# Optimization experiments

Hardware: AMD Instinct MI355X
Metric: run time of the kernel (lower is better)

The kernel has to match this reference:

```python
import jax, jax.numpy as jnp
import numpy as np

SQRT_DK = jnp.sqrt(jnp.float32(128.0))
BN_EPS = 1e-5


def setup_inputs() -> dict:
    key = jax.random.key(0)
    ks = jax.random.split(key, 12)
    B, C, F, Fp, K, O, DK = 4, 64, 20000, 10000, 16, 128, 128
    fea = jax.random.normal(ks[0], (B, C, F), dtype=jnp.float32)
    ring_n = jax.random.randint(ks[1], (B, Fp, K), 0, F, dtype=jnp.int64)
    pool_idx = jnp.sort(jax.random.randint(ks[2], (Fp,), 0, F, dtype=jnp.int64))
    pos_embed = jnp.zeros((1, 1, 1), dtype=jnp.float32)
    s = 1.0 / np.sqrt(C)
    Wk = jax.random.uniform(ks[3], (DK, C), jnp.float32, -s, s)
    bk = jax.random.uniform(ks[4], (DK,), jnp.float32, -s, s)
    Wq = jax.random.uniform(ks[5], (DK, C), jnp.float32, -s, s)
    bq = jax.random.uniform(ks[6], (DK,), jnp.float32, -s, s)
    Wc = jax.random.uniform(ks[7], (O, C), jnp.float32, -s, s)
    bc = jax.random.uniform(ks[8], (O,), jnp.float32, -s, s)
    gamma = jnp.ones((O,), jnp.float32)
    beta = jnp.zeros((O,), jnp.float32)
    return {"fea": fea, "ring_n": ring_n, "pool_idx": pool_idx, "pos_embed": pos_embed,
            "Wk": Wk, "bk": bk, "Wq": Wq, "bq": bq, "Wc": Wc, "bc": bc,
            "gamma": gamma, "beta": beta}


def _gather_neighbors(fea, ring_n):
    # fea: [B,C,F], ring_n: [B,Fp,K] -> [B,C,Fp,K]
    return jax.vmap(lambda f, r: f[:, r])(fea, ring_n)


def reference(fea, ring_n, pool_idx, pos_embed, Wk, bk, Wq, bq, Wc, bc, gamma, beta):
    # neighbor gather along face dim
    neighbor_fea = _gather_neighbors(fea, ring_n)            # [B,C,Fp,K]
    self_fea = fea[:, :, pool_idx][..., None]                # [B,C,Fp,1]
    cat = jnp.concatenate([self_fea, neighbor_fea], axis=3)  # [B,C,Fp,K+1]
    # per-face key (self only) and per-neighbor query (Linear4D over channel dim)
    keyv = jnp.einsum('bcfk,oc->bofk', self_fea, Wk) + bk[None, :, None, None]  # [B,128,Fp,1]
    query = jnp.einsum('bcfk,oc->bofk', cat, Wq) + bq[None, :, None, None]       # [B,128,Fp,K+1]
    att = jnp.sum(keyv * query, axis=1, keepdims=True) / SQRT_DK                 # [B,1,Fp,K+1]
    att = jax.nn.softmax(att, axis=3)
    agg = jnp.sum(cat * att, axis=3)                                             # [B,C,Fp]
    # concat_mlp: 1x1 conv + BatchNorm1d (training-mode batch stats) + ReLU
    y = jnp.einsum('bcf,oc->bof', agg, Wc) + bc[None, :, None]                   # [B,O,Fp]
    mean = jnp.mean(y, axis=(0, 2), keepdims=True)
    var = jnp.var(y, axis=(0, 2), keepdims=True)
    y = (y - mean) * jax.lax.rsqrt(var + BN_EPS)
    y = y * gamma[None, :, None] + beta[None, :, None]
    return jax.nn.relu(y)
```

## Files before the change

kernel.cpp:

```cpp
#include <hip/hip_runtime.h>

#define F_ALL 20000
#define FP    10000
#define BB    4
#define KK    16
#define OO    128
#define NFACE 40000
#define NBLK  625

#define WS_FEAT 0
#define WS_AGG  (BB*F_ALL*64)
#define WS_GP   (WS_AGG + NFACE*64)
#define WS_SAP  (WS_GP + NBLK*4096)
#define WS_MT   (WS_SAP + NBLK*64)
#define WS_V0   (WS_MT + 4096)
#define WS_G    (WS_V0 + 64)
#define WS_SUMA (WS_G + 4096)
#define WS_SC   (WS_SUMA + 64)
#define WS_SH   (WS_SC + 128)

template<int CTRL>
__device__ __forceinline__ float dpp_add(float x) {
    return x + __int_as_float(__builtin_amdgcn_update_dpp(0, __float_as_int(x), CTRL, 0xF, 0xF, true));
}
__device__ __forceinline__ float sum16(float x) {
    x = dpp_add<0x121>(x);
    x = dpp_add<0x122>(x);
    x = dpp_add<0x124>(x);
    x = dpp_add<0x128>(x);
    return x;
}

__device__ __forceinline__ int swz_tile(int bid) {
    int q = bid & 7, s = bid >> 3;
    return (q == 0) ? s : (79 + (q - 1) * 78 + s);
}

__device__ __forceinline__ unsigned int f2bf(float f) {
    unsigned int u = __float_as_uint(f);
    return (u + 0x7FFFu + ((u >> 16) & 1u)) >> 16;
}
__device__ __forceinline__ float b2f(unsigned short h) {
    return __uint_as_float(((unsigned int)h) << 16);
}
__device__ __forceinline__ void up2(unsigned int v, float* d) {
    d[0] = __uint_as_float((v & 0xFFFFu) << 16);
    d[1] = __uint_as_float(v & 0xFFFF0000u);
}

__global__ __launch_bounds__(256) void k_pre(const float* __restrict__ fea,
                                             const float* __restrict__ Wk,
                                             const float* __restrict__ bk,
                                             const float* __restrict__ Wq,
                                             float* __restrict__ ws) {
    __shared__ float tile[64][65];
    int tid = threadIdx.x;
    if (blockIdx.x < 1252) {
        int bb = blockIdx.x / 313;
        int tb = blockIdx.x % 313;
        int fbase = tb * 64;
        int x  = tid & 63;
        int y0 = tid >> 6;
        int f = fbase + x;
        if (f < F_ALL) {
#pragma unroll
            for (int i = 0; i < 16; i++) {
                int c = y0 + i * 4;
                tile[c][x] = fea[((long)bb * 64 + c) * F_ALL + f];
            }
        }
        __syncthreads();
        unsigned int* feaTh = (unsigned int*)(ws + WS_FEAT);
        int xc = (tid & 31) * 2;
        int yr = tid >> 5;
#pragma unroll
        for (int i = 0; i < 8; i++) {
            int fr = yr + i * 8;
            int ff = fbase + fr;
            if (ff < F_ALL) {
                unsigned int lo = f2bf(tile[xc][fr]);
                unsigned int hi = f2bf(tile[xc + 1][fr]);
                feaTh[(long)(bb * F_ALL + ff) * 32 + (tid & 31)] = lo | (hi << 16);
            }
        }
    } else {
        int idx = (blockIdx.x - 1252) * 256 + tid;
        int j = idx >> 6, i = idx & 63;
        float acc = 0.f;
#pragma unroll 8
        for (int o = 0; o < 128; o++) acc += Wq[o * 64 + i] * Wk[o * 64 + j];
        ws[WS_MT + idx] = acc;
        if (blockIdx.x == 1252 && tid < 64) {
            float a = 0.f;
            for (int o = 0; o < 128; o++) a += Wq[o * 64 + tid] * bk[o];
            ws[WS_V0 + tid] = a;
            ws[WS_SUMA + tid] = 0.f;
        }
    }
}

__global__ __launch_bounds__(256) void k_attn(const int* __restrict__ ring,
                                              const int* __restrict__ pool,
                                              float* __restrict__ ws) {
    __shared__ __align__(16) float lds[4160];
    float* Sf = lds;
    int tid = threadIdx.x;
    int tilei = swz_tile(blockIdx.x);
    int fbase = tilei * 64;
    const unsigned short* feaTh = (const unsigned short*)(ws + WS_FEAT);
    const float* MTg  = ws + WS_MT;
    const float scale = 0.08838834764831845f;

    {
        int r = tid >> 2;
        int face = fbase + r;
        int b = face / FP;
        int p = pool[face - b * FP];
        const uint4* src = (const uint4*)(feaTh + ((long)(b * F_ALL + p)) * 64);
        int q = tid & 3;
        uint4 A  = src[q * 2];
        uint4 Bv = src[q * 2 + 1];
        float* d = &Sf[r * 65 + q * 16];
        up2(A.x,  d +  0); up2(A.y,  d +  2); up2(A.z,  d +  4); up2(A.w,  d +  6);
        up2(Bv.x, d +  8); up2(Bv.y, d + 10); up2(Bv.z, d + 12); up2(Bv.w, d + 14);
    }
    __syncthreads();

    int lane = tid & 63;
    int il = lane & 15, c4 = il * 4;
    int f0 = tid >> 4;

    float4 u[4];
    {
        float4 v0 = *(const float4*)&ws[WS_V0 + c4];
        u[0] = v0; u[1] = v0; u[2] = v0; u[3] = v0;
#pragma unroll 8
        for (int j = 0; j < 64; j++) {
            float4 m4 = *(const float4*)&MTg[j * 64 + c4];
            float a0 = Sf[(f0     ) * 65 + j];
            float a1 = Sf[(f0 + 16) * 65 + j];
            float a2 = Sf[(f0 + 32) * 65 + j];
            float a3 = Sf[(f0 + 48) * 65 + j];
            u[0].x += m4.x * a0; u[0].y += m4.y * a0; u[0].z += m4.z * a0; u[0].w += m4.w * a0;
            u[1].x += m4.x * a1; u[1].y += m4.y * a1; u[1].z += m4.z * a1; u[1].w += m4.w * a1;
            u[2].x += m4.x * a2; u[2].y += m4.y * a2; u[2].z += m4.z * a2; u[2].w += m4.w * a2;
            u[3].x += m4.x * a3; u[3].y += m4.y * a3; u[3].z += m4.z * a3; u[3].w += m4.w * a3;
        }
    }

    float4 a_res[4];
#pragma unroll
    for (int it = 0; it < 4; it++) {
        int fl = f0 + it * 16;
        int face = fbase + fl;
        int b = face / FP;
        const unsigned short* fb = feaTh + (long)b * F_ALL * 64 + c4;

        float4 sf = make_float4(Sf[fl * 65 + c4], Sf[fl * 65 + c4 + 1],
                                Sf[fl * 65 + c4 + 2], Sf[fl * 65 + c4 + 3]);
        float4 uu = u[it];
        int rv = ring[face * KK + il];

        float m = sum16(uu.x * sf.x + uu.y * sf.y + uu.z * sf.z + uu.w * sf.w) * scale;
        float den = 1.f;
        float4 acc = sf;
#pragma unroll
        for (int ch = 0; ch < 2; ch++) {
            float4 nv[8];
#pragma unroll
            for (int k = 0; k < 8; k++) {
                int rk = __shfl(rv, (lane & 48) | (ch * 8 + k), 64);
                ushort4 hv = *(const ushort4*)(fb + (long)rk * 64);
                nv[k] = make_float4(b2f(hv.x), b2f(hv.y), b2f(hv.z), b2f(hv.w));
            }
            float l[8];
#pragma unroll
            for (int k = 0; k < 8; k++)
                l[k] = sum16(uu.x * nv[k].x + uu.y * nv[k].y +
                             uu.z * nv[k].z + uu.w * nv[k].w) * scale;
            float cm = l[0];
#pragma unroll
            for (int k = 1; k < 8; k++) cm = fmaxf(cm, l[k]);
            float nm = fmaxf(m, cm);
            float rs = __expf(m - nm);
            den *= rs;
            acc.x *= rs; acc.y *= rs; acc.z *= rs; acc.w *= rs;
            m = nm;
#pragma unroll
            for (int k = 0; k < 8; k++) {
                float e = __expf(l[k] - m);
                den += e;
                acc.x += e * nv[k].x;
                acc.y += e * nv[k].y;
                acc.z += e * nv[k].z;
                acc.w += e * nv[k].w;
            }
        }
        float inv = 1.0f / den;
        float4 a = make_float4(acc.x * inv, acc.y * inv, acc.z * inv, acc.w * inv);
        a_res[it] = a;
        *(float4*)&ws[WS_AGG + (long)face * 64 + c4] = a;
    }
    __syncthreads();
    float* Ag = lds;
#pragma unroll
    for (int it = 0; it < 4; it++) {
        int fl = f0 + it * 16;
        *(float4*)&Ag[fl * 64 + c4] = a_res[it];
    }
    __syncthreads();

    int ti = tid & 15, tj = tid >> 4;
    float acc[4][4];
#pragma unroll
    for (int a = 0; a < 4; a++)
#pragma unroll
        for (int b = 0; b < 4; b++) acc[a][b] = 0.f;
    float gacc[4] = {0.f, 0.f, 0.f, 0.f};
#pragma unroll 4
    for (int f = 0; f < 64; f++) {
        float4 av = *(const float4*)&Ag[f * 64 + ti * 4];
        float4 bv = *(const float4*)&Ag[f * 64 + tj * 4];
        float avv[4] = {av.x, av.y, av.z, av.w};
        float bvv[4] = {bv.x, bv.y, bv.z, bv.w};
#pragma unroll
        for (int a = 0; a < 4; a++) {
#pragma unroll
            for (int b = 0; b < 4; b++) acc[a][b] += avv[a] * bvv[b];
            gacc[a] += avv[a];
        }
    }
    float* gp = ws + WS_GP;
#pragma unroll
    for (int a = 0; a < 4; a++)
        *(float4*)&gp[(long)tilei * 4096 + (ti * 4 + a) * 64 + tj * 4] =
            make_float4(acc[a][0], acc[a][1], acc[a][2], acc[a][3]);
    if (tj == 0)
        *(float4*)&ws[WS_SAP + tilei * 64 + ti * 4] =
            make_float4(gacc[0], gacc[1], gacc[2], gacc[3]);
}

__global__ __launch_bounds__(256) void k_gsum(float* __restrict__ ws) {
    __shared__ float red[256];
    int t = threadIdx.x;
    if (blockIdx.x < 256) {
        const float* gp = ws + WS_GP;
        int e16 = blockIdx.x * 16;
        int e = t & 15, c = t >> 4;
        int p0 = c * 40;
        int p1 = p0 + 40; if (p1 > NBLK) p1 = NBLK;
        float s0 = 0.f, s1 = 0.f, s2 = 0.f, s3 = 0.f;
        int p = p0;
        for (; p + 4 <= p1; p += 4) {
            s0 += gp[(long)(p + 0) * 4096 + e16 + e];
            s1 += gp[(long)(p + 1) * 4096 + e16 + e];
            s2 += gp[(long)(p + 2) * 4096 + e16 + e];
            s3 += gp[(long)(p + 3) * 4096 + e16 + e];
        }
        for (; p < p1; p++) s0 += gp[(long)p * 4096 + e16 + e];
        red[t] = (s0 + s1) + (s2 + s3);
        __syncthreads();
        if (t < 16) {
            float s = 0.f;
#pragma unroll
            for (int cc = 0; cc < 16; cc++) s += red[cc * 16 + t];
            ws[WS_G + e16 + t] = s;
        }
    } else {
        const float* sap = ws + WS_SAP;
        int bq = blockIdx.x - 256;
        int e = t & 63, c = t >> 6;
        int pidx = bq * 4 + c;
        int p0 = pidx * 40;
        int p1 = p0 + 40; if (p1 > NBLK) p1 = NBLK;
        float s0 = 0.f, s1 = 0.f, s2 = 0.f, s3 = 0.f;
        int p = p0;
        for (; p + 4 <= p1; p += 4) {
            s0 += sap[(p + 0) * 64 + e];
            s1 += sap[(p + 1) * 64 + e];
            s2 += sap[(p + 2) * 64 + e];
            s3 += sap[(p + 3) * 64 + e];
        }
        for (; p < p1; p++) s0 += sap[p * 64 + e];
        red[t] = (s0 + s1) + (s2 + s3);
        __syncthreads();
        if (t < 64) {
            float tot = red[t] + red[t + 64] + red[t + 128] + red[t + 192];
            atomicAdd(&ws[WS_SUMA + t], tot);
        }
    }
}

__global__ __launch_bounds__(256) void k_stats(const float* __restrict__ Wc,
                                               const float* __restrict__ bc,
                                               const float* __restrict__ gamma,
                                               const float* __restrict__ beta,
                                               float* __restrict__ ws) {
    __shared__ float Gs[4096];
    __shared__ float gs[64];
    __shared__ float qs[256];
    int tid = threadIdx.x;
    for (int i = tid; i < 4096; i += 256) Gs[i] = ws[WS_G + i];
    if (tid < 64) gs[tid] = ws[WS_SUMA + tid];
    __syncthreads();

    int o = tid & 127, h = tid >> 7;
    float w[64];
#pragma unroll
    for (int q = 0; q < 16; q++) {
        float4 t = *(const float4*)&Wc[o * 64 + q * 4];
        w[q * 4 + 0] = t.x; w[q * 4 + 1] = t.y; w[q * 4 + 2] = t.z; w[q * 4 + 3] = t.w;
    }
    float qp = 0.f;
    for (int i = h * 32; i < h * 32 + 32; i++) {
        float t = 0.f;
#pragma unroll
        for (int j = 0; j < 64; j++) t += Gs[i * 64 + j] * w[j];
        qp += Wc[o * 64 + i] * t;
    }
    qs[tid] = qp;
    __syncthreads();
    if (h == 0) {
        const float invN = 1.0f / (float)NFACE;
        float qform = qs[o] + qs[o + 128];
        float md = 0.f;
#pragma unroll
        for (int j = 0; j < 64; j++) md += gs[j] * w[j];
        float bco = bc[o];
        float mean = md * invN + bco;
        float ey2  = (qform + 2.f * bco * md) * invN + bco * bco;
        float var  = ey2 - mean * mean;
        float sc   = gamma[o] * rsqrtf(var + 1e-5f);
        ws[WS_SC + o] = sc;
        ws[WS_SH + o] = beta[o] + (bco - mean) * sc;
    }
}

__global__ __launch_bounds__(256) void k_out(const float* __restrict__ Wc,
                                             const float* __restrict__ ws,
                                             float* __restrict__ out) {
    __shared__ __align__(16) float WcT[64 * 132];
    __shared__ __align__(16) float AgT[64 * 68];
    const float* agg = ws + WS_AGG;
    int tid = threadIdx.x;
    int fbase = blockIdx.x * 64;
    for (int i = tid; i < 128 * 64; i += 256) {
        int o = i >> 6, j = i & 63;
        WcT[j * 132 + o] = Wc[i];
    }
    for (int i = tid; i < 64 * 64; i += 256) {
        int f = i >> 6, j = i & 63;
        AgT[j * 68 + f] = agg[((long)(fbase + f)) * 64 + j];
    }
    __syncthreads();

    int tx = tid & 15, ty = tid >> 4;
    float acc[8][4];
#pragma unroll
    for (int a = 0; a < 8; a++)
#pragma unroll
        for (int b = 0; b < 4; b++) acc[a][b] = 0.f;

    for (int j = 0; j < 64; j++) {
        float4 w0 = *(const float4*)&WcT[j * 132 + ty * 8];
        float4 w1 = *(const float4*)&WcT[j * 132 + ty * 8 + 4];
        float4 a0 = *(const float4*)&AgT[j * 68 + tx * 4];
        float wv[8] = {w0.x, w0.y, w0.z, w0.w, w1.x, w1.y, w1.z, w1.w};
        float av[4] = {a0.x, a0.y, a0.z, a0.w};
#pragma unroll
        for (int oi = 0; oi < 8; oi++)
#pragma unroll
            for (int fi = 0; fi < 4; fi++) acc[oi][fi] += wv[oi] * av[fi];
    }

    int fg0 = fbase + tx * 4;
    int b   = fg0 / FP;
    int fp0 = fg0 - b * FP;
#pragma unroll
    for (int oi = 0; oi < 8; oi++) {
        int o = ty * 8 + oi;
        float sc = ws[WS_SC + o];
        float sh = ws[WS_SH + o];
        float4 v;
        v.x = fmaxf(acc[oi][0] * sc + sh, 0.f);
        v.y = fmaxf(acc[oi][1] * sc + sh, 0.f);
        v.z = fmaxf(acc[oi][2] * sc + sh, 0.f);
        v.w = fmaxf(acc[oi][3] * sc + sh, 0.f);
        *(float4*)&out[((long)(b * OO + o)) * FP + fp0] = v;
    }
}

extern "C" void kernel_launch(void* const* d_in, const int* in_sizes, int n_in,
                              void* d_out, int out_size, void* d_ws, size_t ws_size,
                              hipStream_t stream) {
    const float* fea  = (const float*)d_in[0];
    const int*   ring = (const int*)d_in[1];
    const int*   pool = (const int*)d_in[2];
    const float* Wk = (const float*)d_in[4];
    const float* bk = (const float*)d_in[5];
    const float* Wq = (const float*)d_in[6];
    const float* Wc = (const float*)d_in[8];
    const float* bc = (const float*)d_in[9];
    const float* gamma = (const float*)d_in[10];
    const float* beta  = (const float*)d_in[11];

    float* out = (float*)d_out;
    float* ws  = (float*)d_ws;

    k_pre  <<<1268, 256, 0, stream>>>(fea, Wk, bk, Wq, ws);
    k_attn <<<NBLK, 256, 0, stream>>>(ring, pool, ws);
    k_gsum <<<260,  256, 0, stream>>>(ws);
    k_stats<<<1,    256, 0, stream>>>(Wc, bc, gamma, beta, ws);
    k_out  <<<NBLK, 256, 0, stream>>>(Wc, ws, out);
}
```

Measured before the change: 165.2 us.

## Fold BN stats into output kernel, stage MT in LDS, prefetch ring indices

Removes the single-block k_stats launch and has every k_out block recompute the BatchNorm scale and shift from the Gram matrix and channel sums, keeping them in shared memory. In k_attn the 64x64 MT matrix is staged into LDS instead of being read from global memory in the inner loop, and the four ring index loads are issued before the barrier so they overlap with the feature staging. The aim is to drop a serial one-block kernel and its launch gap and to cut global traffic in the attention kernel. In exchange each of the 625 output blocks repeats the small quadratic-form computation, and k_attn uses more LDS, which may lower its occupancy.

```diff
diff --git a/kernel.cpp b/kernel.cpp
--- a/kernel.cpp
+++ b/kernel.cpp
@@ -16,8 +16,6 @@
 #define WS_V0   (WS_MT + 4096)
 #define WS_G    (WS_V0 + 64)
 #define WS_SUMA (WS_G + 4096)
-#define WS_SC   (WS_SUMA + 64)
-#define WS_SH   (WS_SC + 128)
 
 template<int CTRL>
 __device__ __forceinline__ float dpp_add(float x) {
@@ -102,15 +100,16 @@
 __global__ __launch_bounds__(256) void k_attn(const int* __restrict__ ring,
                                               const int* __restrict__ pool,
                                               float* __restrict__ ws) {
-    __shared__ __align__(16) float lds[4160];
-    float* Sf = lds;
+    __shared__ __align__(16) float lds[8256];
+    float* Sf  = lds;
+    float* MTl = lds + 4160;
     int tid = threadIdx.x;
     int tilei = swz_tile(blockIdx.x);
     int fbase = tilei * 64;
     const unsigned short* feaTh = (const unsigned short*)(ws + WS_FEAT);
-    const float* MTg  = ws + WS_MT;
     const float scale = 0.08838834764831845f;
 
+    for (int i = tid; i < 4096; i += 256) MTl[i] = ws[WS_MT + i];
     {
         int r = tid >> 2;
         int face = fbase + r;
@@ -124,11 +123,17 @@
         up2(A.x,  d +  0); up2(A.y,  d +  2); up2(A.z,  d +  4); up2(A.w,  d +  6);
         up2(Bv.x, d +  8); up2(Bv.y, d + 10); up2(Bv.z, d + 12); up2(Bv.w, d + 14);
     }
-    __syncthreads();
 
     int lane = tid & 63;
     int il = lane & 15, c4 = il * 4;
     int f0 = tid >> 4;
+
+    int rv4[4];
+#pragma unroll
+    for (int it = 0; it < 4; it++)
+        rv4[it] = ring[(fbase + f0 + it * 16) * KK + il];
+
+    __syncthreads();
 
     float4 u[4];
     {
@@ -136,7 +141,7 @@
         u[0] = v0; u[1] = v0; u[2] = v0; u[3] = v0;
 #pragma unroll 8
         for (int j = 0; j < 64; j++) {
-            float4 m4 = *(const float4*)&MTg[j * 64 + c4];
+            float4 m4 = *(const float4*)&MTl[j * 64 + c4];
             float a0 = Sf[(f0     ) * 65 + j];
             float a1 = Sf[(f0 + 16) * 65 + j];
             float a2 = Sf[(f0 + 32) * 65 + j];
@@ -159,7 +164,7 @@
         float4 sf = make_float4(Sf[fl * 65 + c4], Sf[fl * 65 + c4 + 1],
                                 Sf[fl * 65 + c4 + 2], Sf[fl * 65 + c4 + 3]);
         float4 uu = u[it];
-        int rv = ring[face * KK + il];
+        int rv = rv4[it];
 
         float m = sum16(uu.x * sf.x + uu.y * sf.y + uu.z * sf.z + uu.w * sf.w) * scale;
         float den = 1.f;
@@ -291,58 +296,59 @@
     }
 }
 
-__global__ __launch_bounds__(256) void k_stats(const float* __restrict__ Wc,
-                                               const float* __restrict__ bc,
-                                               const float* __restrict__ gamma,
-                                               const float* __restrict__ beta,
-                                               float* __restrict__ ws) {
-    __shared__ float Gs[4096];
-    __shared__ float gs[64];
-    __shared__ float qs[256];
-    int tid = threadIdx.x;
-    for (int i = tid; i < 4096; i += 256) Gs[i] = ws[WS_G + i];
-    if (tid < 64) gs[tid] = ws[WS_SUMA + tid];
-    __syncthreads();
-
-    int o = tid & 127, h = tid >> 7;
-    float w[64];
-#pragma unroll
-    for (int q = 0; q < 16; q++) {
-        float4 t = *(const float4*)&Wc[o * 64 + q * 4];
-        w[q * 4 + 0] = t.x; w[q * 4 + 1] = t.y; w[q * 4 + 2] = t.z; w[q * 4 + 3] = t.w;
-    }
-    float qp = 0.f;
-    for (int i = h * 32; i < h * 32 + 32; i++) {
-        float t = 0.f;
-#pragma unroll
-        for (int j = 0; j < 64; j++) t += Gs[i * 64 + j] * w[j];
-        qp += Wc[o * 64 + i] * t;
-    }
-    qs[tid] = qp;
-    __syncthreads();
-    if (h == 0) {
-        const float invN = 1.0f / (float)NFACE;
-        float qform = qs[o] + qs[o + 128];
-        float md = 0.f;
-#pragma unroll
-        for (int j = 0; j < 64; j++) md += gs[j] * w[j];
-        float bco = bc[o];
-        float mean = md * invN + bco;
-        float ey2  = (qform + 2.f * bco * md) * invN + bco * bco;
-        float var  = ey2 - mean * mean;
-        float sc   = gamma[o] * rsqrtf(var + 1e-5f);
-        ws[WS_SC + o] = sc;
-        ws[WS_SH + o] = beta[o] + (bco - mean) * sc;
-    }
-}
-
 __global__ __launch_bounds__(256) void k_out(const float* __restrict__ Wc,
+                                             const float* __restrict__ bc,
+                                             const float* __restrict__ gamma,
+                                             const float* __restrict__ beta,
                                              const float* __restrict__ ws,
                                              float* __restrict__ out) {
-    __shared__ __align__(16) float WcT[64 * 132];
-    __shared__ __align__(16) float AgT[64 * 68];
+    __shared__ __align__(16) float lds[13056];
+    int tid = threadIdx.x;
+
+    {
+        float* Gs = lds;
+        float* gs = lds + 4096;
+        float* qs = lds + 4160;
+        for (int i = tid; i < 4096; i += 256) Gs[i] = ws[WS_G + i];
+        if (tid < 64) gs[tid] = ws[WS_SUMA + tid];
+        __syncthreads();
+
+        int o = tid & 127, h = tid >> 7;
+        float w[64];
+#pragma unroll
+        for (int q = 0; q < 16; q++) {
+            float4 t = *(const float4*)&Wc[o * 64 + q * 4];
+            w[q * 4 + 0] = t.x; w[q * 4 + 1] = t.y; w[q * 4 + 2] = t.z; w[q * 4 + 3] = t.w;
+        }
+        float qp = 0.f;
+        for (int i = h * 32; i < h * 32 + 32; i++) {
+            float t = 0.f;
+#pragma unroll
+            for (int j = 0; j < 64; j++) t += Gs[i * 64 + j] * w[j];
+            qp += Wc[o * 64 + i] * t;
+        }
+        qs[tid] = qp;
+        __syncthreads();
+        if (h == 0) {
+            const float invN = 1.0f / (float)NFACE;
+            float qform = qs[o] + qs[o + 128];
+            float md = 0.f;
+#pragma unroll
+            for (int j = 0; j < 64; j++) md += gs[j] * w[j];
+            float bco = bc[o];
+            float mean = md * invN + bco;
+            float ey2  = (qform + 2.f * bco * md) * invN + bco * bco;
+            float var  = ey2 - mean * mean;
+            float sc   = gamma[o] * rsqrtf(var + 1e-5f);
+            lds[12800 + o] = sc;
+            lds[12928 + o] = beta[o] + (bco - mean) * sc;
+        }
+        __syncthreads();
+    }
+
+    float* AgT = lds;
+    float* WcT = lds + 4352;
     const float* agg = ws + WS_AGG;
-    int tid = threadIdx.x;
     int fbase = blockIdx.x * 64;
     for (int i = tid; i < 128 * 64; i += 256) {
         int o = i >> 6, j = i & 63;
@@ -379,8 +385,8 @@
 #pragma unroll
     for (int oi = 0; oi < 8; oi++) {
         int o = ty * 8 + oi;
-        float sc = ws[WS_SC + o];
-        float sh = ws[WS_SH + o];
+        float sc = lds[12800 + o];
+        float sh = lds[12928 + o];
         float4 v;
         v.x = fmaxf(acc[oi][0] * sc + sh, 0.f);
         v.y = fmaxf(acc[oi][1] * sc + sh, 0.f);
@@ -410,6 +416,5 @@
     k_pre  <<<1268, 256, 0, stream>>>(fea, Wk, bk, Wq, ws);
     k_attn <<<NBLK, 256, 0, stream>>>(ring, pool, ws);
     k_gsum <<<260,  256, 0, stream>>>(ws);
-    k_stats<<<1,    256, 0, stream>>>(Wc, bc, gamma, beta, ws);
-    k_out  <<<NBLK, 256, 0, stream>>>(Wc, ws, out);
-}
+    k_out  <<<NBLK, 256, 0, stream>>>(Wc, bc, gamma, beta, ws, out);
+}
```

Result: slower. 169.6 us (+2.6%).
